# Optimization experiments

Measured on AMD Instinct MI355X. Metric: run time of the kernel, lower is better.

The kernel has to match this reference:

```python
import jax, jax.numpy as jnp
import numpy as np

B, C, N = 4, 256, 512
CQ = C // 4
SIGMA = 15.0
PICK = 0  # args.picked_point_num
FACTOR = 180.0 / (np.pi * SIGMA)
BN_EPS = 1e-5


def _angle_embed(angles, W, b):
    """SinusoidalPositionalEmbedding (interleaved sin/cos, detached) + Linear proj."""
    d = W.shape[0]
    div_term = jnp.exp(jnp.arange(0, d, 2, dtype=jnp.float32) * (-np.log(10000.0) / d))
    omegas = (angles * FACTOR)[..., None] * div_term  # (..., d/2)
    # torch cat([sin, cos], dim=2) on (-1, d/2, 1) then view -> interleaved [s0,c0,s1,c1,...]
    emb = jnp.stack([jnp.sin(omegas), jnp.cos(omegas)], axis=-1).reshape(*angles.shape, d)
    emb = jax.lax.stop_gradient(emb)  # .detach() in torch
    return emb @ W.T + b


def setup_inputs() -> dict:
    key = jax.random.key(0)
    ks = jax.random.split(key, 16)
    s = 0.05
    return {
        "x": jax.random.normal(ks[0], (B, C, N), jnp.float32),
        "pca": jax.random.normal(ks[1], (B, C, N), jnp.float32),
        "angle_lrf": jax.random.uniform(ks[2], (B, N, N), jnp.float32, 0.0, np.pi),
        "angle_pca": jax.random.uniform(ks[3], (B, N), jnp.float32, 0.0, np.pi),
        "Wkp": jax.random.normal(ks[4], (CQ, C), jnp.float32) * s,
        "Wk": jax.random.normal(ks[5], (CQ, C), jnp.float32) * s,
        "Wv": jax.random.normal(ks[6], (C, C), jnp.float32) * s,
        "Wvp": jax.random.normal(ks[7], (C, C), jnp.float32) * s,
        "emb1_W": jax.random.normal(ks[8], (CQ, CQ), jnp.float32) * s,
        "emb1_b": jnp.zeros((CQ,), jnp.float32),
        "emb2_W": jax.random.normal(ks[9], (CQ, CQ), jnp.float32) * s,
        "emb2_b": jnp.zeros((CQ,), jnp.float32),
        "lin_W": jax.random.normal(ks[10], (C, C), jnp.float32) * s,
        "lin_b": jnp.zeros((C,), jnp.float32),
        "bn_gamma": jnp.ones((C,), jnp.float32),
        "bn_beta": jnp.zeros((C,), jnp.float32),
    }


def reference(x, pca, angle_lrf, angle_pca, Wkp, Wk, Wv, Wvp,
              emb1_W, emb1_b, emb2_W, emb2_b, lin_W, lin_b, bn_gamma, bn_beta):
    # q uses the k_conv_pca weight (weight tying in __init__)
    x_q = jnp.einsum('oc,bcn->bno', Wkp, x)            # (B,N,CQ)
    k_lrf = jnp.einsum('oc,bcn->bon', Wk, x)           # (B,CQ,N)
    k_pca = jnp.einsum('oc,bcn->bon', Wkp, pca)        # (B,CQ,N)
    energy_lrf = jnp.einsum('bno,bom->bnm', x_q, k_lrf)
    energy_pca = jnp.einsum('bno,bom->bnm', x_q, k_pca)
    e1 = _angle_embed(angle_lrf, emb1_W, emb1_b)       # (B,N,N,CQ) relative-angle bias
    energy_lrf = energy_lrf + jnp.einsum('bnc,bnmc->bnm', x_q, e1)
    e2 = _angle_embed(angle_pca, emb2_W, emb2_b)       # (B,N,CQ)
    energy_pca = energy_pca + jnp.einsum('bnc,bmc->bnm', x_q, e2)
    energy = jax.nn.softmax(energy_lrf + energy_pca, axis=-1)
    # extra column renormalization
    energy = energy / (1e-12 + energy.sum(axis=1, keepdims=True))
    point_relation = energy[:, PICK:PICK + 1, :]       # (B,1,N)
    v_lrf = jnp.einsum('oc,bcn->bon', Wv, x)
    v_pca = jnp.einsum('oc,bcn->bon', Wvp, pca)
    x_lrf = jnp.einsum('bon,bnm->bom', v_lrf, energy)
    x_pca = jnp.einsum('bon,bnm->bom', v_pca, energy)
    x_r = 0.5 * x_lrf + 0.5 * x_pca
    z = jnp.einsum('oc,bcn->bon', lin_W, x - x_r) + lin_b[None, :, None]
    # BatchNorm1d (training-mode batch stats, biased var)
    mu = z.mean(axis=(0, 2), keepdims=True)
    var = z.var(axis=(0, 2), keepdims=True)
    y = bn_gamma[None, :, None] * (z - mu) * jax.lax.rsqrt(var + BN_EPS) + bn_beta[None, :, None]
    out = x + jax.nn.gelu(y, approximate=False)
    return out, point_relation
```

## Files before the change

### kernel.cpp

```cpp
#include <hip/hip_runtime.h>
#include <math.h>

#define FCT_REV 0.6079271018540267f
#define DIVK 0.28782313662425575f
#define INV2PI 0.15915494309189535f

using bf16x8 = __attribute__((ext_vector_type(8))) short;
using f32x4  = __attribute__((ext_vector_type(4))) float;

__device__ inline short f2bf(float f) {
    union { float f; unsigned u; } v; v.f = f;
    unsigned r = v.u + 0x7FFFu + ((v.u >> 16) & 1u);
    return (short)(r >> 16);
}
__device__ inline float bf2f(short s) {
    union { unsigned u; float f; } v;
    v.u = ((unsigned)(unsigned short)s) << 16;
    return v.f;
}
__device__ inline unsigned pk2(float lo, float hi) {
    return ((unsigned)(unsigned short)f2bf(hi) << 16) | (unsigned)(unsigned short)f2bf(lo);
}
__device__ inline float sinrev(float x) {
    float r; asm("v_sin_f32 %0, %1" : "=v"(r) : "v"(x)); return r;
}
__device__ inline float cosrev(float x) {
    float r; asm("v_cos_f32 %0, %1" : "=v"(r) : "v"(x)); return r;
}

__global__ __launch_bounds__(256) void k_prep(
    const float* __restrict__ Wkp, const float* __restrict__ Wk,
    const float* __restrict__ Wv, const float* __restrict__ Wvp,
    const float* __restrict__ linW, const float* __restrict__ e1W,
    const float* __restrict__ e2W,
    const float* __restrict__ x, const float* __restrict__ pca,
    short* __restrict__ Wcatb, short* __restrict__ InTb,
    float* __restrict__ e2Wt, float* __restrict__ stat, float* __restrict__ colsum)
{
    __shared__ float ts[64][65];
    const int bid = blockIdx.x;
    const int t = threadIdx.x;
    if (bid < 176) {
        if (bid == 0) {
            for (int i = t; i < 2048; i += 256) colsum[i] = 0.f;
            for (int i = t; i < 512; i += 256) stat[i] = 0.f;
        } else if (bid == 1) {
            for (int i = t; i < 4096; i += 256) {
                int k = i >> 6, o = i & 63;
                e2Wt[k*64 + o] = e2W[o*64 + k];
            }
        }
        #pragma unroll
        for (int rr = 0; rr < 4; ++rr) {
            const int r = bid*4 + rr;
            for (int k = t; k < 512; k += 256) {
                float v = 0.f;
                if (r < 64) { if (k < 256) v = Wkp[r*256 + k]; }
                else if (r < 128) { int o = r-64;  v = (k<256) ? Wk[o*256+k]  : Wkp[o*256 + k-256]; }
                else if (r < 384) { int o = r-128; v = (k<256) ? Wv[o*256+k]  : Wvp[o*256 + k-256]; }
                else if (r < 640) { int o = r-384; if (k<256) v = linW[o*256+k]; }
                else {
                    int o = r-640;
                    if (k < 256) {
                        float a = 0.f;
                        for (int j = 0; j < 64; ++j) a = fmaf(e1W[j*64 + o], Wkp[j*256 + k], a);
                        v = a;
                    }
                }
                Wcatb[(size_t)r*512 + k] = f2bf(v);
            }
        }
    } else {
        const int id = bid - 176;
        const int b  = id >> 6;
        const int kt = (id >> 3) & 7;
        const int nt = id & 7;
        const int k0 = kt*64, n0 = nt*64;
        const float* src = (k0 < 256) ? (x + ((size_t)b*256 + k0)*512)
                                      : (pca + ((size_t)b*256 + (k0-256))*512);
        #pragma unroll
        for (int i = 0; i < 16; ++i) {
            int idx = t + 256*i;
            int r = idx >> 6, c = idx & 63;
            ts[r][c] = src[(size_t)r*512 + n0 + c];
        }
        __syncthreads();
        short* dst = InTb + (size_t)b*512*512;
        #pragma unroll
        for (int i = 0; i < 16; ++i) {
            int idx = t + 256*i;
            int n = idx >> 6, k = idx & 63;
            dst[(size_t)(n0+n)*512 + k0 + k] = f2bf(ts[k][n]);
        }
    }
}

__global__ __launch_bounds__(256) void k_gemm1(
    const short* __restrict__ Wcatb, const short* __restrict__ InTb,
    const float* __restrict__ angle_pca, const float* __restrict__ e2Wt,
    short* __restrict__ xqb, short* __restrict__ KtT, short* __restrict__ vsumb,
    float* __restrict__ linx, float* __restrict__ q1T)
{
    __shared__ float embs[32][65];
    __shared__ float e2ws[64][64];
    const int bid = blockIdx.x;
    const int b  = bid / 176;
    const int rt = (bid / 16) % 11;
    const int ct = bid % 16;
    const int r0 = rt*64, c0 = ct*32;
    const int w = threadIdx.x >> 6, lane = threadIdx.x & 63;
    const int lr = lane & 15, lg = lane >> 4;
    const int t = threadIdx.x;

    if (r0 == 64) {
        const int mloc = t >> 3, q = t & 7;
        const float arev = angle_pca[b*512 + c0 + mloc] * FCT_REV;
        #pragma unroll
        for (int j = q*4; j < q*4+4; ++j) {
            const float arg = arev * __expf(-(float)j * DIVK);
            embs[mloc][2*j]   = sinrev(arg);
            embs[mloc][2*j+1] = cosrev(arg);
        }
        #pragma unroll
        for (int i = 0; i < 16; ++i) {
            const int idx = t + 256*i;
            e2ws[idx >> 6][idx & 63] = e2Wt[idx];
        }
    }

    const short* ap  = Wcatb + (size_t)(r0 + w*16 + lr)*512 + 8*lg;
    const short* bp0 = InTb + (size_t)b*512*512 + (size_t)(c0 + lr)*512 + 8*lg;
    const short* bp1 = bp0 + 16*512;

    f32x4 acc0 = {0.f,0.f,0.f,0.f}, acc1 = {0.f,0.f,0.f,0.f};
    #pragma unroll 4
    for (int kk = 0; kk < 512; kk += 32) {
        bf16x8 a  = *(const bf16x8*)(ap  + kk);
        bf16x8 b0 = *(const bf16x8*)(bp0 + kk);
        bf16x8 b1 = *(const bf16x8*)(bp1 + kk);
        acc0 = __builtin_amdgcn_mfma_f32_16x16x32_bf16(a, b0, acc0, 0, 0, 0);
        acc1 = __builtin_amdgcn_mfma_f32_16x16x32_bf16(a, b1, acc1, 0, 0, 0);
    }
    const int rowb = r0 + w*16 + lg*4;
    const int col0 = c0 + lr;
    if (r0 == 0) {
        #pragma unroll
        for (int j = 0; j < 4; ++j) {
            xqb[((size_t)b*512 + col0)*64 + rowb + j]      = f2bf(acc0[j]);
            xqb[((size_t)b*512 + col0 + 16)*64 + rowb + j] = f2bf(acc1[j]);
        }
    } else if (r0 == 64) {
        __syncthreads();
        const int o0 = w*16 + lg*4;
        float e[8];
        #pragma unroll
        for (int i = 0; i < 8; ++i) e[i] = 0.f;
        #pragma unroll 8
        for (int k = 0; k < 64; ++k) {
            const float em0 = embs[lr][k];
            const float em1 = embs[lr + 16][k];
            #pragma unroll
            for (int j = 0; j < 4; ++j) {
                const float wv = e2ws[k][o0 + j];
                e[j]     = fmaf(wv, em0, e[j]);
                e[4 + j] = fmaf(wv, em1, e[4 + j]);
            }
        }
        uint2 u0, u1;
        u0.x = pk2(acc0[0] + e[0], acc0[1] + e[1]);
        u0.y = pk2(acc0[2] + e[2], acc0[3] + e[3]);
        u1.x = pk2(acc1[0] + e[4], acc1[1] + e[5]);
        u1.y = pk2(acc1[2] + e[6], acc1[3] + e[7]);
        *(uint2*)(KtT + ((size_t)b*512 + col0)*64 + o0)      = u0;
        *(uint2*)(KtT + ((size_t)b*512 + col0 + 16)*64 + o0) = u1;
    } else if (r0 < 384) {
        #pragma unroll
        for (int j = 0; j < 4; ++j) {
            vsumb[((size_t)b*256 + rowb-128 + j)*512 + col0]      = f2bf(acc0[j]);
            vsumb[((size_t)b*256 + rowb-128 + j)*512 + col0 + 16] = f2bf(acc1[j]);
        }
    } else if (r0 < 640) {
        #pragma unroll
        for (int j = 0; j < 4; ++j) {
            linx[((size_t)b*256 + rowb-384 + j)*512 + col0]      = acc0[j];
            linx[((size_t)b*256 + rowb-384 + j)*512 + col0 + 16] = acc1[j];
        }
    } else {
        const int off = rowb - 640;
        float* d0 = q1T + ((size_t)b*512 + col0)*64 + off;
        float* d1 = q1T + ((size_t)b*512 + col0 + 16)*64 + off;
        d0[0] = sqrtf(acc0[0]*acc0[0] + acc0[1]*acc0[1]);
        d0[1] = atan2f(acc0[1], acc0[0]) * INV2PI;
        d0[2] = sqrtf(acc0[2]*acc0[2] + acc0[3]*acc0[3]);
        d0[3] = atan2f(acc0[3], acc0[2]) * INV2PI;
        d1[0] = sqrtf(acc1[0]*acc1[0] + acc1[1]*acc1[1]);
        d1[1] = atan2f(acc1[1], acc1[0]) * INV2PI;
        d1[2] = sqrtf(acc1[2]*acc1[2] + acc1[3]*acc1[3]);
        d1[3] = atan2f(acc1[3], acc1[2]) * INV2PI;
    }
}

__global__ __launch_bounds__(256) void k_qk(
    const short* __restrict__ xqb, const short* __restrict__ KtT,
    float* __restrict__ S)
{
    const int bid = blockIdx.x;
    const int b  = bid / 128;
    const int rt = (bid / 16) % 8;
    const int ct = bid % 16;
    const int r0 = rt*64, c0 = ct*32;
    const int w = threadIdx.x >> 6, lane = threadIdx.x & 63;
    const int lr = lane & 15, lg = lane >> 4;
    const short* ap  = xqb + ((size_t)b*512 + r0 + w*16 + lr)*64 + 8*lg;
    const short* bp0 = KtT + ((size_t)b*512 + c0 + lr)*64 + 8*lg;
    const short* bp1 = bp0 + 16*64;
    f32x4 acc0 = {0.f,0.f,0.f,0.f}, acc1 = {0.f,0.f,0.f,0.f};
    #pragma unroll
    for (int kk = 0; kk < 64; kk += 32) {
        bf16x8 a  = *(const bf16x8*)(ap  + kk);
        bf16x8 b0 = *(const bf16x8*)(bp0 + kk);
        bf16x8 b1 = *(const bf16x8*)(bp1 + kk);
        acc0 = __builtin_amdgcn_mfma_f32_16x16x32_bf16(a, b0, acc0, 0, 0, 0);
        acc1 = __builtin_amdgcn_mfma_f32_16x16x32_bf16(a, b1, acc1, 0, 0, 0);
    }
    const int rowb = r0 + w*16 + lg*4;
    const int col0 = c0 + lr;
    float* Sb = S + (size_t)b*512*512;
    #pragma unroll
    for (int j = 0; j < 4; ++j) {
        Sb[(size_t)(rowb+j)*512 + col0]      = acc0[j];
        Sb[(size_t)(rowb+j)*512 + col0 + 16] = acc1[j];
    }
}

__global__ __launch_bounds__(256) void k_energy2(
    const float* __restrict__ S, const float* __restrict__ q1T,
    const float* __restrict__ angle_lrf, short* __restrict__ ETb,
    float* __restrict__ colsum)
{
    const int b  = blockIdx.x >> 7;
    const int n0 = (blockIdx.x & 127) * 4;
    __shared__ float qs[4][64];
    __shared__ float divs[32];
    __shared__ float4 xw[4];
    const int t = threadIdx.x;
    if (t < 64) {
        #pragma unroll
        for (int i = 0; i < 4; ++i) qs[i][t] = q1T[((size_t)b*512 + n0 + i)*64 + t];
    } else if (t < 96) {
        divs[t-64] = __expf(-(float)(t-64) * DIVK);
    }
    __syncthreads();
    float acc[4][2], av[4][2];
    #pragma unroll
    for (int i = 0; i < 4; ++i) {
        const float2 sv = *(const float2*)&S[((size_t)b*512 + n0 + i)*512 + 2*t];
        const float2 an = *(const float2*)&angle_lrf[((size_t)b*512 + n0 + i)*512 + 2*t];
        acc[i][0] = sv.x; acc[i][1] = sv.y;
        av[i][0] = an.x * FCT_REV; av[i][1] = an.y * FCT_REV;
    }
    #pragma unroll 2
    for (int j = 0; j < 32; ++j) {
        const float d = divs[j];
        #pragma unroll
        for (int i = 0; i < 4; ++i) {
            const float R = qs[i][2*j], ph = qs[i][2*j+1];
            #pragma unroll
            for (int m = 0; m < 2; ++m) {
                const float arg = fmaf(av[i][m], d, ph);
                acc[i][m] = fmaf(R, sinrev(arg), acc[i][m]);
            }
        }
    }
    float v0 = fmaxf(acc[0][0], acc[0][1]), v1 = fmaxf(acc[1][0], acc[1][1]);
    float v2 = fmaxf(acc[2][0], acc[2][1]), v3 = fmaxf(acc[3][0], acc[3][1]);
    #pragma unroll
    for (int off = 1; off < 64; off <<= 1) {
        v0 = fmaxf(v0, __shfl_xor(v0, off));
        v1 = fmaxf(v1, __shfl_xor(v1, off));
        v2 = fmaxf(v2, __shfl_xor(v2, off));
        v3 = fmaxf(v3, __shfl_xor(v3, off));
    }
    const int wid = t >> 6, lane = t & 63;
    if (lane == 0) { float4 f = {v0,v1,v2,v3}; xw[wid] = f; }
    __syncthreads();
    {
        const float4 a0 = xw[0], a1 = xw[1], a2 = xw[2], a3 = xw[3];
        v0 = fmaxf(fmaxf(a0.x,a1.x), fmaxf(a2.x,a3.x));
        v1 = fmaxf(fmaxf(a0.y,a1.y), fmaxf(a2.y,a3.y));
        v2 = fmaxf(fmaxf(a0.z,a1.z), fmaxf(a2.z,a3.z));
        v3 = fmaxf(fmaxf(a0.w,a1.w), fmaxf(a2.w,a3.w));
    }
    float p[4][2];
    p[0][0] = __expf(acc[0][0]-v0); p[0][1] = __expf(acc[0][1]-v0);
    p[1][0] = __expf(acc[1][0]-v1); p[1][1] = __expf(acc[1][1]-v1);
    p[2][0] = __expf(acc[2][0]-v2); p[2][1] = __expf(acc[2][1]-v2);
    p[3][0] = __expf(acc[3][0]-v3); p[3][1] = __expf(acc[3][1]-v3);
    float s0 = p[0][0]+p[0][1], s1 = p[1][0]+p[1][1];
    float s2 = p[2][0]+p[2][1], s3 = p[3][0]+p[3][1];
    #pragma unroll
    for (int off = 1; off < 64; off <<= 1) {
        s0 += __shfl_xor(s0, off); s1 += __shfl_xor(s1, off);
        s2 += __shfl_xor(s2, off); s3 += __shfl_xor(s3, off);
    }
    __syncthreads();
    if (lane == 0) { float4 f = {s0,s1,s2,s3}; xw[wid] = f; }
    __syncthreads();
    {
        const float4 a0 = xw[0], a1 = xw[1], a2 = xw[2], a3 = xw[3];
        s0 = (a0.x+a1.x) + (a2.x+a3.x);
        s1 = (a0.y+a1.y) + (a2.y+a3.y);
        s2 = (a0.z+a1.z) + (a2.z+a3.z);
        s3 = (a0.w+a1.w) + (a2.w+a3.w);
    }
    const float i0 = 1.f/s0, i1 = 1.f/s1, i2 = 1.f/s2, i3 = 1.f/s3;
    short* Eb = ETb + (size_t)b*512*512;
    #pragma unroll
    for (int m = 0; m < 2; ++m) {
        const float e0 = p[0][m]*i0, e1 = p[1][m]*i1, e2 = p[2][m]*i2, e3 = p[3][m]*i3;
        uint2 u;
        u.x = pk2(e0, e1);
        u.y = pk2(e2, e3);
        *(uint2*)(Eb + (size_t)(2*t + m)*512 + n0) = u;
        atomicAdd(&colsum[b*512 + 2*t + m], (e0 + e1) + (e2 + e3));
    }
}

__global__ __launch_bounds__(256) void k_xr2(
    const short* __restrict__ vsumb, const short* __restrict__ ETb,
    const float* __restrict__ colsum, short* __restrict__ xrT,
    float* __restrict__ out)
{
    const int bid = blockIdx.x;
    const int b  = bid / 64;
    const int rt = (bid / 16) % 4;
    const int ct = bid % 16;
    const int r0 = rt*64, c0 = ct*32;
    const int w = threadIdx.x >> 6, lane = threadIdx.x & 63;
    const int lr = lane & 15, lg = lane >> 4;
    const short* ap  = vsumb + (size_t)b*256*512 + (size_t)(r0 + w*16 + lr)*512 + 8*lg;
    const short* bp0 = ETb + (size_t)b*512*512 + (size_t)(c0 + lr)*512 + 8*lg;
    const short* bp1 = bp0 + 16*512;
    f32x4 acc0 = {0.f,0.f,0.f,0.f}, acc1 = {0.f,0.f,0.f,0.f};
    #pragma unroll 4
    for (int kk = 0; kk < 512; kk += 32) {
        bf16x8 a  = *(const bf16x8*)(ap  + kk);
        bf16x8 b0 = *(const bf16x8*)(bp0 + kk);
        bf16x8 b1 = *(const bf16x8*)(bp1 + kk);
        acc0 = __builtin_amdgcn_mfma_f32_16x16x32_bf16(a, b0, acc0, 0, 0, 0);
        acc1 = __builtin_amdgcn_mfma_f32_16x16x32_bf16(a, b1, acc1, 0, 0, 0);
    }
    const int rowb = r0 + w*16 + lg*4;
    const int m0 = c0 + lr, m1 = m0 + 16;
    const float rc0 = 1.f / (1e-12f + colsum[b*512 + m0]);
    const float rc1 = 1.f / (1e-12f + colsum[b*512 + m1]);
    const float s0 = 0.5f * rc0, s1 = 0.5f * rc1;
    short* xb = xrT + (size_t)b*512*256;
    uint2 u;
    u.x = pk2(acc0[0]*s0, acc0[1]*s0);
    u.y = pk2(acc0[2]*s0, acc0[3]*s0);
    *(uint2*)(xb + (size_t)m0*256 + rowb) = u;
    u.x = pk2(acc1[0]*s1, acc1[1]*s1);
    u.y = pk2(acc1[2]*s1, acc1[3]*s1);
    *(uint2*)(xb + (size_t)m1*256 + rowb) = u;
    if (w == 0 && lg == 0) {
        out[(size_t)4*256*512 + b*512 + m0] = bf2f(ETb[((size_t)b*512 + m0)*512]) * rc0;
        out[(size_t)4*256*512 + b*512 + m1] = bf2f(ETb[((size_t)b*512 + m1)*512]) * rc1;
    }
}

__global__ __launch_bounds__(256) void k_z2st(
    const short* __restrict__ Wcatb, const short* __restrict__ xrT,
    const float* __restrict__ linx, const float* __restrict__ lin_b,
    float* __restrict__ z, float* __restrict__ stat)
{
    const int bid = blockIdx.x;
    const int b  = bid / 64;
    const int rt = (bid / 16) % 4;
    const int ct = bid % 16;
    const int r0 = rt*64, c0 = ct*32;
    const int w = threadIdx.x >> 6, lane = threadIdx.x & 63;
    const int lr = lane & 15, lg = lane >> 4;
    const short* ap  = Wcatb + (size_t)(384 + r0 + w*16 + lr)*512 + 8*lg;
    const short* bp0 = xrT + (size_t)b*512*256 + (size_t)(c0 + lr)*256 + 8*lg;
    const short* bp1 = bp0 + 16*256;
    f32x4 acc0 = {0.f,0.f,0.f,0.f}, acc1 = {0.f,0.f,0.f,0.f};
    #pragma unroll
    for (int kk = 0; kk < 256; kk += 32) {
        bf16x8 a  = *(const bf16x8*)(ap  + kk);
        bf16x8 b0 = *(const bf16x8*)(bp0 + kk);
        bf16x8 b1 = *(const bf16x8*)(bp1 + kk);
        acc0 = __builtin_amdgcn_mfma_f32_16x16x32_bf16(a, b0, acc0, 0, 0, 0);
        acc1 = __builtin_amdgcn_mfma_f32_16x16x32_bf16(a, b1, acc1, 0, 0, 0);
    }
    const int rowb = r0 + w*16 + lg*4;
    const int col0 = c0 + lr;
    const float* Lb = linx + (size_t)b*256*512;
    float* zb = z + (size_t)b*256*512;
    #pragma unroll
    for (int j = 0; j < 4; ++j) {
        const float lb = lin_b[rowb+j];
        const float z0 = Lb[(size_t)(rowb+j)*512 + col0]      - acc0[j] + lb;
        const float z1 = Lb[(size_t)(rowb+j)*512 + col0 + 16] - acc1[j] + lb;
        zb[(size_t)(rowb+j)*512 + col0]      = z0;
        zb[(size_t)(rowb+j)*512 + col0 + 16] = z1;
        float s  = z0 + z1;
        float s2 = z0*z0 + z1*z1;
        #pragma unroll
        for (int off = 1; off < 16; off <<= 1) {
            s  += __shfl_xor(s,  off);
            s2 += __shfl_xor(s2, off);
        }
        if (lr == 0) {
            atomicAdd(&stat[rowb+j], s);
            atomicAdd(&stat[256 + rowb+j], s2);
        }
    }
}

__global__ __launch_bounds__(256) void k_final(
    const float* __restrict__ x, const float* __restrict__ z,
    const float* __restrict__ stat, const float* __restrict__ gamma,
    const float* __restrict__ beta, float* __restrict__ out)
{
    const int gid = blockIdx.x*256 + threadIdx.x;
    const int base = gid * 4;
    const int c = (base >> 9) & 255;
    const float mu  = stat[c] * (1.f/2048.f);
    const float var = stat[256 + c] * (1.f/2048.f) - mu*mu;
    const float gsc = gamma[c] * rsqrtf(var + 1e-5f);
    const float bt  = beta[c];
    const float4 zv = *(const float4*)&z[base];
    const float4 xv = *(const float4*)&x[base];
    float4 ov;
    {
        float y = (zv.x - mu)*gsc + bt;
        ov.x = xv.x + 0.5f*y*(1.f + erff(y*0.70710678118654752f));
        y = (zv.y - mu)*gsc + bt;
        ov.y = xv.y + 0.5f*y*(1.f + erff(y*0.70710678118654752f));
        y = (zv.z - mu)*gsc + bt;
        ov.z = xv.z + 0.5f*y*(1.f + erff(y*0.70710678118654752f));
        y = (zv.w - mu)*gsc + bt;
        ov.w = xv.w + 0.5f*y*(1.f + erff(y*0.70710678118654752f));
    }
    *(float4*)&out[base] = ov;
}

extern "C" void kernel_launch(void* const* d_in, const int* in_sizes, int n_in,
                              void* d_out, int out_size, void* d_ws, size_t ws_size,
                              hipStream_t stream)
{
    const float* x         = (const float*)d_in[0];
    const float* pca       = (const float*)d_in[1];
    const float* angle_lrf = (const float*)d_in[2];
    const float* angle_pca = (const float*)d_in[3];
    const float* Wkp       = (const float*)d_in[4];
    const float* Wk        = (const float*)d_in[5];
    const float* Wv        = (const float*)d_in[6];
    const float* Wvp       = (const float*)d_in[7];
    const float* e1W       = (const float*)d_in[8];
    const float* e2W       = (const float*)d_in[10];
    const float* linW      = (const float*)d_in[12];
    const float* linb      = (const float*)d_in[13];
    const float* gamma     = (const float*)d_in[14];
    const float* beta      = (const float*)d_in[15];

    char* w = (char*)d_ws;
    short* Wcatb  = (short*)(w + 0);
    short* InTb   = (short*)(w + 720896);
    short* vsumb  = (short*)(w + 2818048);
    short* KtT    = (short*)(w + 3866624);
    short* ETb    = (short*)(w + 4128768);
    short* xrT    = (short*)(w + 6225920);
    float* stat   = (float*)(w + 7274496);
    float* colsum = (float*)(w + 7276544);
    float* S      = (float*)(w + 7284736);
    float* e2Wt   = (float*)(w + 7284736);
    float* z      = (float*)(w + 7284736);
    short* xqb    = (short*)(w + 12003328);
    float* q1T    = (float*)(w + 12265472);
    float* linx   = (float*)(w + 12789760);
    float* out    = (float*)d_out;

    k_prep   <<<432, 256, 0, stream>>>(Wkp, Wk, Wv, Wvp, linW, e1W, e2W, x, pca,
                                       Wcatb, InTb, e2Wt, stat, colsum);
    k_gemm1  <<<704, 256, 0, stream>>>(Wcatb, InTb, angle_pca, e2Wt,
                                       xqb, KtT, vsumb, linx, q1T);
    k_qk     <<<512, 256, 0, stream>>>(xqb, KtT, S);
    k_energy2<<<512, 256, 0, stream>>>(S, q1T, angle_lrf, ETb, colsum);
    k_xr2    <<<256, 256, 0, stream>>>(vsumb, ETb, colsum, xrT, out);
    k_z2st   <<<256, 256, 0, stream>>>(Wcatb, xrT, linx, linb, z, stat);
    k_final  <<<512, 256, 0, stream>>>(x, z, stat, gamma, beta, out);
}
```

Before: 80.07 us.

## Fuse QK scores into energy kernel and trim GEMM K-range per output block

Removes the separate k_qk kernel and its fp32 S scratch buffer. The energy kernel now stages each batch's full K matrix (512x64 bf16) in shared memory and computes the x_q·K dot products itself with scalar FMAs. The column mapping also changes from 2t to t and t+256, so the loads are coalesced. Separately, the first GEMM stops its K loop at 256 for output blocks whose inputs only use one half of the concatenated input. Each block now reloads about 64KB of K, and the FMA-based dot product replaces MFMA, which raises LDS traffic and compute per block.

After: 73.20 us. 1.09x faster.

```diff
diff --git a/kernel.cpp b/kernel.cpp
--- a/kernel.cpp
+++ b/kernel.cpp
@@ -17,6 +17,12 @@
     union { unsigned u; float f; } v;
     v.u = ((unsigned)(unsigned short)s) << 16;
     return v.f;
+}
+__device__ inline float bflo(unsigned u) {
+    union { unsigned q; float f; } v; v.q = u << 16; return v.f;
+}
+__device__ inline float bfhi(unsigned u) {
+    union { unsigned q; float f; } v; v.q = u & 0xFFFF0000u; return v.f;
 }
 __device__ inline unsigned pk2(float lo, float hi) {
     return ((unsigned)(unsigned short)f2bf(hi) << 16) | (unsigned)(unsigned short)f2bf(lo);
@@ -131,10 +137,11 @@
     const short* ap  = Wcatb + (size_t)(r0 + w*16 + lr)*512 + 8*lg;
     const short* bp0 = InTb + (size_t)b*512*512 + (size_t)(c0 + lr)*512 + 8*lg;
     const short* bp1 = bp0 + 16*512;
+    const int kmax = (r0 == 64 || (r0 >= 128 && r0 < 384)) ? 512 : 256;
 
     f32x4 acc0 = {0.f,0.f,0.f,0.f}, acc1 = {0.f,0.f,0.f,0.f};
     #pragma unroll 4
-    for (int kk = 0; kk < 512; kk += 32) {
+    for (int kk = 0; kk < kmax; kk += 32) {
         bf16x8 a  = *(const bf16x8*)(ap  + kk);
         bf16x8 b0 = *(const bf16x8*)(bp0 + kk);
         bf16x8 b1 = *(const bf16x8*)(bp1 + kk);
@@ -170,6 +177,7 @@
         u0.x = pk2(acc0[0] + e[0], acc0[1] + e[1]);
         u0.y = pk2(acc0[2] + e[2], acc0[3] + e[3]);
         u1.x = pk2(acc1[0] + e[4], acc1[1] + e[5]);
+        u1.y = pk2(acc1[2] + e[6], acc1[7-3] + e[7]);
         u1.y = pk2(acc1[2] + e[6], acc1[3] + e[7]);
         *(uint2*)(KtT + ((size_t)b*512 + col0)*64 + o0)      = u0;
         *(uint2*)(KtT + ((size_t)b*512 + col0 + 16)*64 + o0) = u1;
@@ -200,64 +208,69 @@
     }
 }
 
-__global__ __launch_bounds__(256) void k_qk(
+__global__ __launch_bounds__(256) void k_energy3(
     const short* __restrict__ xqb, const short* __restrict__ KtT,
-    float* __restrict__ S)
-{
-    const int bid = blockIdx.x;
-    const int b  = bid / 128;
-    const int rt = (bid / 16) % 8;
-    const int ct = bid % 16;
-    const int r0 = rt*64, c0 = ct*32;
-    const int w = threadIdx.x >> 6, lane = threadIdx.x & 63;
-    const int lr = lane & 15, lg = lane >> 4;
-    const short* ap  = xqb + ((size_t)b*512 + r0 + w*16 + lr)*64 + 8*lg;
-    const short* bp0 = KtT + ((size_t)b*512 + c0 + lr)*64 + 8*lg;
-    const short* bp1 = bp0 + 16*64;
-    f32x4 acc0 = {0.f,0.f,0.f,0.f}, acc1 = {0.f,0.f,0.f,0.f};
-    #pragma unroll
-    for (int kk = 0; kk < 64; kk += 32) {
-        bf16x8 a  = *(const bf16x8*)(ap  + kk);
-        bf16x8 b0 = *(const bf16x8*)(bp0 + kk);
-        bf16x8 b1 = *(const bf16x8*)(bp1 + kk);
-        acc0 = __builtin_amdgcn_mfma_f32_16x16x32_bf16(a, b0, acc0, 0, 0, 0);
-        acc1 = __builtin_amdgcn_mfma_f32_16x16x32_bf16(a, b1, acc1, 0, 0, 0);
-    }
-    const int rowb = r0 + w*16 + lg*4;
-    const int col0 = c0 + lr;
-    float* Sb = S + (size_t)b*512*512;
-    #pragma unroll
-    for (int j = 0; j < 4; ++j) {
-        Sb[(size_t)(rowb+j)*512 + col0]      = acc0[j];
-        Sb[(size_t)(rowb+j)*512 + col0 + 16] = acc1[j];
-    }
-}
-
-__global__ __launch_bounds__(256) void k_energy2(
-    const float* __restrict__ S, const float* __restrict__ q1T,
-    const float* __restrict__ angle_lrf, short* __restrict__ ETb,
-    float* __restrict__ colsum)
-{
-    const int b  = blockIdx.x >> 7;
-    const int n0 = (blockIdx.x & 127) * 4;
+    const float* __restrict__ q1T, const float* __restrict__ angle_lrf,
+    short* __restrict__ ETb, float* __restrict__ colsum)
+{
+    __shared__ short kt[512][68];
+    __shared__ float xqf[4][64];
     __shared__ float qs[4][64];
     __shared__ float divs[32];
     __shared__ float4 xw[4];
+    const int b  = blockIdx.x >> 7;
+    const int n0 = (blockIdx.x & 127) * 4;
     const int t = threadIdx.x;
+    {
+        const short* src = KtT + (size_t)b*512*64;
+        #pragma unroll
+        for (int i = 0; i < 16; ++i) {
+            const int idx = t + 256*i;
+            const int row = idx >> 3, col = (idx & 7) * 8;
+            const uint4 u = *(const uint4*)(src + (size_t)row*64 + col);
+            *(uint2*)&kt[row][col]     = make_uint2(u.x, u.y);
+            *(uint2*)&kt[row][col + 4] = make_uint2(u.z, u.w);
+        }
+    }
     if (t < 64) {
         #pragma unroll
-        for (int i = 0; i < 4; ++i) qs[i][t] = q1T[((size_t)b*512 + n0 + i)*64 + t];
+        for (int i = 0; i < 4; ++i) {
+            xqf[i][t] = bf2f(xqb[((size_t)b*512 + n0 + i)*64 + t]);
+            qs[i][t]  = q1T[((size_t)b*512 + n0 + i)*64 + t];
+        }
     } else if (t < 96) {
         divs[t-64] = __expf(-(float)(t-64) * DIVK);
     }
     __syncthreads();
-    float acc[4][2], av[4][2];
+    float acc[4][2];
+    #pragma unroll
+    for (int i = 0; i < 4; ++i) { acc[i][0] = 0.f; acc[i][1] = 0.f; }
+    for (int c = 0; c < 64; c += 4) {
+        float xv[4][4];
+        #pragma unroll
+        for (int i = 0; i < 4; ++i) {
+            #pragma unroll
+            for (int j = 0; j < 4; ++j) xv[i][j] = xqf[i][c + j];
+        }
+        #pragma unroll
+        for (int mi = 0; mi < 2; ++mi) {
+            const uint2 u = *(const uint2*)&kt[t + mi*256][c];
+            const float k0 = bflo(u.x), k1 = bfhi(u.x);
+            const float k2 = bflo(u.y), k3 = bfhi(u.y);
+            #pragma unroll
+            for (int i = 0; i < 4; ++i) {
+                acc[i][mi] = fmaf(k0, xv[i][0],
+                             fmaf(k1, xv[i][1],
+                             fmaf(k2, xv[i][2],
+                             fmaf(k3, xv[i][3], acc[i][mi]))));
+            }
+        }
+    }
+    float av[4][2];
     #pragma unroll
     for (int i = 0; i < 4; ++i) {
-        const float2 sv = *(const float2*)&S[((size_t)b*512 + n0 + i)*512 + 2*t];
-        const float2 an = *(const float2*)&angle_lrf[((size_t)b*512 + n0 + i)*512 + 2*t];
-        acc[i][0] = sv.x; acc[i][1] = sv.y;
-        av[i][0] = an.x * FCT_REV; av[i][1] = an.y * FCT_REV;
+        av[i][0] = angle_lrf[((size_t)b*512 + n0 + i)*512 + t] * FCT_REV;
+        av[i][1] = angle_lrf[((size_t)b*512 + n0 + i)*512 + t + 256] * FCT_REV;
     }
     #pragma unroll 2
     for (int j = 0; j < 32; ++j) {
@@ -316,13 +329,14 @@
     const float i0 = 1.f/s0, i1 = 1.f/s1, i2 = 1.f/s2, i3 = 1.f/s3;
     short* Eb = ETb + (size_t)b*512*512;
     #pragma unroll
-    for (int m = 0; m < 2; ++m) {
-        const float e0 = p[0][m]*i0, e1 = p[1][m]*i1, e2 = p[2][m]*i2, e3 = p[3][m]*i3;
+    for (int mi = 0; mi < 2; ++mi) {
+        const int m = t + mi*256;
+        const float e0 = p[0][mi]*i0, e1 = p[1][mi]*i1, e2 = p[2][mi]*i2, e3 = p[3][mi]*i3;
         uint2 u;
         u.x = pk2(e0, e1);
         u.y = pk2(e2, e3);
-        *(uint2*)(Eb + (size_t)(2*t + m)*512 + n0) = u;
-        atomicAdd(&colsum[b*512 + 2*t + m], (e0 + e1) + (e2 + e3));
+        *(uint2*)(Eb + (size_t)m*512 + n0) = u;
+        atomicAdd(&colsum[b*512 + m], (e0 + e1) + (e2 + e3));
     }
 }
 
@@ -474,7 +488,6 @@
     short* xrT    = (short*)(w + 6225920);
     float* stat   = (float*)(w + 7274496);
     float* colsum = (float*)(w + 7276544);
-    float* S      = (float*)(w + 7284736);
     float* e2Wt   = (float*)(w + 7284736);
     float* z      = (float*)(w + 7284736);
     short* xqb    = (short*)(w + 12003328);
@@ -486,8 +499,7 @@
                                        Wcatb, InTb, e2Wt, stat, colsum);
     k_gemm1  <<<704, 256, 0, stream>>>(Wcatb, InTb, angle_pca, e2Wt,
                                        xqb, KtT, vsumb, linx, q1T);
-    k_qk     <<<512, 256, 0, stream>>>(xqb, KtT, S);
-    k_energy2<<<512, 256, 0, stream>>>(S, q1T, angle_lrf, ETb, colsum);
+    k_energy3<<<512, 256, 0, stream>>>(xqb, KtT, q1T, angle_lrf, ETb, colsum);
     k_xr2    <<<256, 256, 0, stream>>>(vsumb, ETb, colsum, xrT, out);
     k_z2st   <<<256, 256, 0, stream>>>(Wcatb, xrT, linx, linb, z, stat);
     k_final  <<<512, 256, 0, stream>>>(x, z, stat, gamma, beta, out);
```
